# Optimization experiments

Hardware: AMD Instinct MI355X
Metric: run time of the kernel (lower is better)

## Reference

```python
import math
import jax, jax.numpy as jnp
import numpy as np

B, S, D, H = 2, 2048, 2048, 16
HD = D // H  # head_dim = 128


def setup_inputs() -> dict:
    key = jax.random.key(0)
    ks = jax.random.split(key, 5)
    x = jax.random.normal(ks[0], (B, S, D), dtype=jnp.float32)
    # torch nn.Linear weights are [out_features, in_features]
    wq = jax.random.normal(ks[1], (D, D), dtype=jnp.float32) * 0.02
    wk = jax.random.normal(ks[2], (D, D), dtype=jnp.float32) * 0.02
    wv = jax.random.normal(ks[3], (D, D), dtype=jnp.float32) * 0.02
    wo = jax.random.normal(ks[4], (D, D), dtype=jnp.float32) * 0.02
    # llama-style rotary frequencies: freq_cis[t, i] = exp(1j * t / 10000^(2i/hd))
    inv_freq = 1.0 / (10000.0 ** (jnp.arange(0, HD, 2, dtype=jnp.float32) / HD))  # [HD/2]
    angles = jnp.arange(S, dtype=jnp.float32)[:, None] * inv_freq[None, :]  # [S, HD/2]
    freq_cos = jnp.cos(angles)
    freq_sin = jnp.sin(angles)
    # additive causal mask (0 on/below diagonal, large negative above)
    mask = jnp.triu(jnp.full((S, S), -1e9, dtype=jnp.float32), k=1)
    return {"x": x, "wq": wq, "wk": wk, "wv": wv, "wo": wo,
            "freq_cos": freq_cos, "freq_sin": freq_sin, "mask": mask}


def _rope(t, cos, sin):
    # t: [B, H, S, HD]; cos/sin: [S, HD/2]. Consecutive pairs form complex numbers.
    b, h, s, hd = t.shape
    tr = t.reshape(b, h, s, hd // 2, 2)
    re, im = tr[..., 0], tr[..., 1]
    c = cos[None, None, :, :]
    sn = sin[None, None, :, :]
    out_re = re * c - im * sn
    out_im = re * sn + im * c
    return jnp.stack([out_re, out_im], axis=-1).reshape(b, h, s, hd)


def reference(x, wq, wk, wv, wo, freq_cos, freq_sin, mask):
    b, s, d = x.shape
    hd = 2 * freq_cos.shape[-1]
    h = wq.shape[0] // hd
    # projections (torch Linear: y = x @ W.T)
    q = jnp.einsum('bsd,ed->bse', x, wq).reshape(b, s, h, hd).transpose(0, 2, 1, 3)
    k = jnp.einsum('bsd,ed->bse', x, wk).reshape(b, s, h, hd).transpose(0, 2, 1, 3)
    v = jnp.einsum('bsd,ed->bse', x, wv).reshape(b, s, h, hd).transpose(0, 2, 1, 3)
    q = _rope(q, freq_cos, freq_sin)
    k = _rope(k, freq_cos, freq_sin)
    scores = jnp.einsum('bhqd,bhkd->bhqk', q, k) / math.sqrt(hd)  # [B,H,S,S]
    scores = scores + mask[None, None, :, :]
    attn = jax.nn.softmax(scores, axis=-1)
    o = jnp.einsum('bhqk,bhkd->bhqd', attn, v)
    o = o.transpose(0, 2, 1, 3).reshape(b, s, h * hd)
    return jnp.einsum('bse,de->bsd', o, wo)
```

## Files before the change

### kernel.cpp

```cpp
#include <hip/hip_runtime.h>
#include <stdint.h>

#define BB  2
#define SS  2048
#define DD  2048
#define HH  16
#define HDD 128
#define MM  (BB * SS)

typedef __attribute__((ext_vector_type(8)))  short short8;
typedef __attribute__((ext_vector_type(4)))  float f32x4;
typedef __attribute__((ext_vector_type(16))) float f32x16;
typedef unsigned int   u32;
typedef unsigned short u16;
typedef __attribute__((ext_vector_type(4))) u16 u16x4;
typedef __attribute__((ext_vector_type(2))) u32 u32x2;
typedef __attribute__((ext_vector_type(4))) u32 u32x4;

static __device__ __forceinline__ u16 f2bf(float f) {
  u32 u = __builtin_bit_cast(u32, f);
  u32 r = u + 0x7fffu + ((u >> 16) & 1u);
  return (u16)(r >> 16);
}

static __device__ __forceinline__ u32 cvtpk(float a, float b) {
  u32 r;
  asm("v_cvt_pk_bf16_f32 %0, %1, %2" : "=v"(r) : "v"(a), "v"(b));
  return r;
}
static __device__ __forceinline__ void permswap(u32& a, u32& b) {
  asm volatile("v_permlane32_swap_b32 %0, %1" : "+v"(a), "+v"(b));
}

__global__ void cvt_all(const float* __restrict__ x,  const float* __restrict__ wq,
                        const float* __restrict__ wk, const float* __restrict__ wv,
                        const float* __restrict__ wo,
                        u16* __restrict__ xb, u16* __restrict__ wqkv,
                        u16* __restrict__ wob) {
  const int NX = (MM * DD) / 4;
  const int NW = (DD * DD) / 4;
  const int total = NX + 4 * NW;
  for (int i = blockIdx.x * blockDim.x + threadIdx.x; i < total;
       i += gridDim.x * blockDim.x) {
    const float* s; u16* d; int off;
    if (i < NX) { s = x; d = xb; off = i; }
    else {
      int j = i - NX; int w = j >> 20; off = j & (NW - 1);
      s = (w == 0) ? wq : (w == 1) ? wk : (w == 2) ? wv : wo;
      d = (w < 3) ? (wqkv + (size_t)w * DD * DD) : wob;
    }
    f32x4 v = *(const f32x4*)(s + (size_t)off * 4);
    u16x4 o;
#pragma unroll
    for (int j = 0; j < 4; ++j) o[j] = f2bf(v[j]);
    *(u16x4*)(d + (size_t)off * 4) = o;
  }
}

__global__ __launch_bounds__(256) void gemm_qkv(const u16* __restrict__ A,
                                                const u16* __restrict__ Bw,
                                                u16* __restrict__ Cq,
                                                u16* __restrict__ Ck,
                                                u16* __restrict__ Cvt,
                                                const float* __restrict__ fc,
                                                const float* __restrict__ fs) {
  const int K = DD;
  __shared__ __align__(16) u16 Al[128 * 64];
  __shared__ __align__(16) u16 Bl[128 * 64];
  const int tid  = threadIdx.x;
  const int wave = tid >> 6, lane = tid & 63;
  const int m0 = blockIdx.y * 128, n0 = blockIdx.x * 128;
  const int wr = (wave >> 1) * 64, wc = (wave & 1) * 64;
  const int lrow = lane & 15, kh = lane >> 4;
  const int sk = lrow & 7;

  f32x4 acc[4][4] = {};

#define GSTAGE(T)                                                                       \
  {                                                                                     \
    int koff = (T) * 64;                                                                \
    _Pragma("unroll")                                                                   \
    for (int j_ = 0; j_ < 4; ++j_) {                                                    \
      int i_ = tid + j_ * 256;                                             \
      int r_ = i_ >> 3, c_ = i_ & 7;                                                    \
      int sc_ = (c_ ^ (r_ & 7)) * 8;                                                    \
      const u16* ga = A  + (size_t)(m0 + r_) * K + koff + sc_;                          \
      __builtin_amdgcn_global_load_lds((const __attribute__((address_space(1))) u32*)ga,\
                                       (__attribute__((address_space(3))) u32*)(Al + i_ * 8), \
                                       16, 0, 0);                                       \
      const u16* gb = Bw + (size_t)(n0 + r_) * K + koff + sc_;                          \
      __builtin_amdgcn_global_load_lds((const __attribute__((address_space(1))) u32*)gb,\
                                       (__attribute__((address_space(3))) u32*)(Bl + i_ * 8), \
                                       16, 0, 0);                                       \
    }                                                                                   \
  }

  const int NT = K / 64;
  for (int t = 0; t < NT; ++t) {
    if (t) __syncthreads();
    GSTAGE(t);
    __syncthreads();

    short8 af[4][2], bf[4][2];
#pragma unroll
    for (int tt = 0; tt < 4; ++tt)
#pragma unroll
      for (int ks = 0; ks < 2; ++ks) {
        af[tt][ks] = *(const short8*)(Al + (wr + tt * 16 + lrow) * 64 + ((ks * 4 + kh) ^ sk) * 8);
        bf[tt][ks] = *(const short8*)(Bl + (wc + tt * 16 + lrow) * 64 + ((ks * 4 + kh) ^ sk) * 8);
      }
#pragma unroll
    for (int mt = 0; mt < 4; ++mt)
#pragma unroll
      for (int nt = 0; nt < 4; ++nt)
#pragma unroll
        for (int ks = 0; ks < 2; ++ks)
          acc[mt][nt] = __builtin_amdgcn_mfma_f32_16x16x32_bf16(af[mt][ks], bf[nt][ks], acc[mt][nt], 0, 0, 0);
  }
#undef GSTAGE

  const int dr = kh * 4;
  const int region = n0 >> 11;
  if (region < 2) {
    u16* Cd = region ? Ck : Cq;
    const float sfac = region ? 1.f : 0.08838834764831845f * 1.44269504088896340736f;
#pragma unroll
    for (int mt = 0; mt < 4; ++mt)
#pragma unroll
      for (int nt = 0; nt < 4; ++nt) {
        int c  = n0 + wc + nt * 16 + lrow;
        int cl = c & 2047;
        int dh = cl & 127, pi = dh >> 1;
        float sgn = (dh & 1) ? 1.f : -1.f;
#pragma unroll
        for (int i = 0; i < 4; ++i) {
          int r  = m0 + wr + mt * 16 + dr + i;
          int s_ = r & (SS - 1);
          float cc_ = fc[s_ * 64 + pi] * sfac;
          float ss_ = fs[s_ * 64 + pi] * (sgn * sfac);
          float v  = acc[mt][nt][i];
          float pv = __shfl_xor(v, 1, 64);
          Cd[(size_t)r * 2048 + cl] = f2bf(v * cc_ + pv * ss_);
        }
      }
  } else {
#pragma unroll
    for (int mt = 0; mt < 4; ++mt)
#pragma unroll
      for (int nt = 0; nt < 4; ++nt) {
        int cl = (n0 - 4096) + wc + nt * 16 + lrow;
        int rr = m0 + wr + mt * 16 + dr;
        int b  = rr >> 11, s0 = rr & 2047;
        u16x4 pk;
#pragma unroll
        for (int i = 0; i < 4; ++i) pk[i] = f2bf(acc[mt][nt][i]);
        *(u16x4*)(Cvt + ((size_t)b * 2048 + cl) * 2048 + s0) = pk;
      }
  }
}

__global__ __launch_bounds__(256) void gemm_o_db(const u16* __restrict__ A,
                                                 const u16* __restrict__ Bw,
                                                 float* __restrict__ Cf,
                                                 int M, int N, int K) {
  __shared__ __align__(16) u16 Al[2][128 * 64];
  __shared__ __align__(16) u16 Bl[2][128 * 64];
  const int tid  = threadIdx.x;
  const int wave = tid >> 6, lane = tid & 63;
  const int m0 = blockIdx.y * 128, n0 = blockIdx.x * 128;
  const int wr = (wave >> 1) * 64, wc = (wave & 1) * 64;
  const int lrow = lane & 15, kh = lane >> 4;
  const int sk = lrow & 7;

  f32x4 acc[4][4] = {};

#define GSTAGE(T, BUF)                                                                  \
  {                                                                                     \
    int koff = (T) * 64;                                                                \
    _Pragma("unroll")                                                                   \
    for (int j_ = 0; j_ < 4; ++j_) {                                                    \
      int i_ = tid + j_ * 256;                                                          \
      int r_ = i_ >> 3, c_ = i_ & 7;                                                    \
      int sc_ = (c_ ^ (r_ & 7)) * 8;                                                    \
      const u16* ga = A  + (size_t)(m0 + r_) * K + koff + sc_;                          \
      __builtin_amdgcn_global_load_lds((const __attribute__((address_space(1))) u32*)ga,\
                                       (__attribute__((address_space(3))) u32*)(&Al[BUF][0] + i_ * 8), \
                                       16, 0, 0);                                       \
      const u16* gb = Bw + (size_t)(n0 + r_) * K + koff + sc_;                          \
      __builtin_amdgcn_global_load_lds((const __attribute__((address_space(1))) u32*)gb,\
                                       (__attribute__((address_space(3))) u32*)(&Bl[BUF][0] + i_ * 8), \
                                       16, 0, 0);                                       \
    }                                                                                   \
  }

  const int NT = K / 64;
  GSTAGE(0, 0);
  for (int t = 0; t < NT; ++t) {
    const int bt = t & 1;
    if (t + 1 < NT) {
      GSTAGE(t + 1, bt ^ 1);
      asm volatile("s_waitcnt vmcnt(8)" ::: "memory");
    } else {
      asm volatile("s_waitcnt vmcnt(0)" ::: "memory");
    }
    __builtin_amdgcn_s_barrier();

    const u16* Ab = &Al[bt][0];
    const u16* Bb = &Bl[bt][0];
    short8 af[4][2], bf[4][2];
#pragma unroll
    for (int tt = 0; tt < 4; ++tt)
#pragma unroll
      for (int ks = 0; ks < 2; ++ks) {
        af[tt][ks] = *(const short8*)(Ab + (wr + tt * 16 + lrow) * 64 + ((ks * 4 + kh) ^ sk) * 8);
        bf[tt][ks] = *(const short8*)(Bb + (wc + tt * 16 + lrow) * 64 + ((ks * 4 + kh) ^ sk) * 8);
      }
#pragma unroll
    for (int mt = 0; mt < 4; ++mt)
#pragma unroll
      for (int nt = 0; nt < 4; ++nt)
#pragma unroll
        for (int ks = 0; ks < 2; ++ks)
          acc[mt][nt] = __builtin_amdgcn_mfma_f32_16x16x32_bf16(af[mt][ks], bf[nt][ks], acc[mt][nt], 0, 0, 0);

    __builtin_amdgcn_s_barrier();
  }
#undef GSTAGE

  const int dr = kh * 4;
#pragma unroll
  for (int mt = 0; mt < 4; ++mt)
#pragma unroll
    for (int nt = 0; nt < 4; ++nt)
#pragma unroll
      for (int i = 0; i < 4; ++i) {
        size_t r = (size_t)(m0 + wr + mt * 16 + dr + i);
        size_t c = (size_t)(n0 + wc + nt * 16 + lrow);
        Cf[r * N + c] = acc[mt][nt][i];
      }
}

__global__ __launch_bounds__(256, 2) void attn_kernel(const u16* __restrict__ Q,
                                                      const u16* __restrict__ K,
                                                      const u16* __restrict__ Vt,
                                                      u16* __restrict__ O) {
  __shared__ __align__(16) u16 Kl[2][64 * 128];
  __shared__ __align__(16) u16 Vl[2][128 * 64];

  const int tid = threadIdx.x, wave = tid >> 6, lane = tid & 63;
  const int l31 = lane & 31, hi = lane >> 5;
  const int bh = blockIdx.x, b = bh >> 4, h = bh & 15;
  const int y = blockIdx.y;
  const int qt = (y < 8) ? y : (23 - y);
  const size_t base    = ((size_t)b * SS) * DD + (size_t)h * HDD;
  const size_t vt_base = (size_t)bh * HDD * SS;
  const int swz = (l31 & 7) << 4;

#define STAGE(KT, BUF)                                                              \
  {                                                                                 \
    int k0s = (KT) * 64;                                                            \
    _Pragma("unroll")                                                               \
    for (int i_ = 0; i_ < 4; ++i_) {                                                \
      int idx = tid + i_ * 256;                                                     \
      int kr = idx >> 4, c_ = idx & 15;                                             \
      const u16* gk = K + base + (size_t)(k0s + kr) * DD + ((c_ ^ (kr & 7)) * 8);   \
      __builtin_amdgcn_global_load_lds((const __attribute__((address_space(1))) u32*)gk, \
                                       (__attribute__((address_space(3))) u32*)(&Kl[BUF][0] + idx * 8), \
                                       16, 0, 0);                                   \
      int dv = idx >> 3, c2 = idx & 7;                                              \
      const u16* gv = Vt + vt_base + (size_t)dv * SS + k0s + ((c2 ^ (dv & 7)) * 8); \
      __builtin_amdgcn_global_load_lds((const __attribute__((address_space(1))) u32*)gv, \
                                       (__attribute__((address_space(3))) u32*)(&Vl[BUF][0] + idx * 8), \
                                       16, 0, 0);                                   \
    }                                                                               \
  }

  const int qw = qt * 128 + wave * 32;
  const int q_ = qw + l31;

  short8 qf[8];
#pragma unroll
  for (int kc = 0; kc < 8; ++kc)
    qf[kc] = *(const short8*)(Q + base + (size_t)(qw + l31) * DD + kc * 16 + hi * 8);

  f32x16 oacc[4] = {};
  float m_i = -1e30f, l_p = 0.f;

  int buf = 0;
  STAGE(0, 0);

  const int ntiles = 2 * qt + 2;
  for (int kt = 0; kt < ntiles; ++kt) {
    const int k0 = kt * 64;
    if (kt + 1 < ntiles) {
      STAGE(kt + 1, buf ^ 1);
      asm volatile("s_waitcnt vmcnt(8)" ::: "memory");
    } else {
      asm volatile("s_waitcnt vmcnt(0)" ::: "memory");
    }
    __builtin_amdgcn_s_barrier();

    if (k0 <= qw + 31) {
      const u16* Kb_ = &Kl[buf][0];
      const u16* Vb_ = &Vl[buf][0];

      f32x16 st[2] = {};
      __builtin_amdgcn_s_setprio(1);
#pragma unroll
      for (int kc = 0; kc < 8; ++kc) {
        int by0 = (l31 * 256)        + ((kc * 32 + hi * 16) ^ swz);
        int by1 = ((32 + l31) * 256) + ((kc * 32 + hi * 16) ^ swz);
        short8 a0 = *(const short8*)(Kb_ + (by0 >> 1));
        short8 a1 = *(const short8*)(Kb_ + (by1 >> 1));
        st[0] = __builtin_amdgcn_mfma_f32_32x32x16_bf16(a0, qf[kc], st[0], 0, 0, 0);
        st[1] = __builtin_amdgcn_mfma_f32_32x32x16_bf16(a1, qf[kc], st[1], 0, 0, 0);
      }
      __builtin_amdgcn_s_setprio(0);

      float mx = -1e30f;
      if (k0 + 63 > qw) {
#pragma unroll
        for (int kb = 0; kb < 2; ++kb)
#pragma unroll
          for (int r = 0; r < 16; ++r) {
            float s = st[kb][r];
            int key = k0 + kb * 32 + (r & 3) + ((r >> 2) << 3) + (hi << 2);
            if (key > q_) s = -1e30f;
            st[kb][r] = s;
            mx = fmaxf(mx, s);
          }
      } else {
#pragma unroll
        for (int kb = 0; kb < 2; ++kb)
#pragma unroll
          for (int r = 0; r < 16; ++r) mx = fmaxf(mx, st[kb][r]);
      }
      mx = fmaxf(mx, __shfl_xor(mx, 32, 64));

      if (__any(mx > m_i + 8.f)) {
        float mn  = fmaxf(m_i, mx);
        float esc = exp2f(m_i - mn);
        m_i = mn; l_p *= esc;
#pragma unroll
        for (int db = 0; db < 4; ++db)
#pragma unroll
          for (int r = 0; r < 16; ++r) oacc[db][r] *= esc;
      }
      float sum = 0.f;
#pragma unroll
      for (int kb = 0; kb < 2; ++kb)
#pragma unroll
        for (int r = 0; r < 16; ++r) {
          float e = exp2f(st[kb][r] - m_i);
          st[kb][r] = e;
          sum += e;
        }
      l_p += sum;

      __builtin_amdgcn_s_setprio(1);
#pragma unroll
      for (int kb = 0; kb < 2; ++kb) {
#pragma unroll
        for (int half = 0; half < 2; ++half) {
          const int rb = half * 8;
          u32 w0 = cvtpk(st[kb][rb + 0], st[kb][rb + 1]);
          u32 w1 = cvtpk(st[kb][rb + 2], st[kb][rb + 3]);
          u32 w2 = cvtpk(st[kb][rb + 4], st[kb][rb + 5]);
          u32 w3 = cvtpk(st[kb][rb + 6], st[kb][rb + 7]);
          permswap(w0, w2);
          permswap(w1, w3);
          short8 pf = __builtin_bit_cast(short8, (u32x4){w0, w1, w2, w3});
          const int ktv = kb * 2 + half;
#pragma unroll
          for (int db = 0; db < 4; ++db) {
            int d = db * 32 + l31;
            int by = d * 128 + ((ktv * 32 + hi * 16) ^ swz);
            short8 vf = *(const short8*)(Vb_ + (by >> 1));
            oacc[db] = __builtin_amdgcn_mfma_f32_32x32x16_bf16(vf, pf, oacc[db], 0, 0, 0);
          }
        }
      }
      __builtin_amdgcn_s_setprio(0);
    }
    __builtin_amdgcn_s_barrier();
    buf ^= 1;
  }

  float lt  = l_p + __shfl_xor(l_p, 32, 64);
  float inv = 1.f / lt;
#pragma unroll
  for (int db = 0; db < 4; ++db)
#pragma unroll
    for (int g = 0; g < 4; ++g) {
      int d0 = db * 32 + 8 * g + 4 * hi;
      u32x2 pk;
      pk[0] = cvtpk(oacc[db][4 * g + 0] * inv, oacc[db][4 * g + 1] * inv);
      pk[1] = cvtpk(oacc[db][4 * g + 2] * inv, oacc[db][4 * g + 3] * inv);
      *(u32x2*)(O + base + (size_t)q_ * DD + d0) = pk;
    }
#undef STAGE
}

extern "C" void kernel_launch(void* const* d_in, const int* in_sizes, int n_in,
                              void* d_out, int out_size, void* d_ws, size_t ws_size,
                              hipStream_t stream) {
  (void)in_sizes; (void)n_in; (void)out_size; (void)ws_size;
  const float* x  = (const float*)d_in[0];
  const float* wq = (const float*)d_in[1];
  const float* wk = (const float*)d_in[2];
  const float* wv = (const float*)d_in[3];
  const float* wo = (const float*)d_in[4];
  const float* fc = (const float*)d_in[5];
  const float* fs = (const float*)d_in[6];
  float* out = (float*)d_out;

  const size_t XBUF = (size_t)MM * DD * 2;
  const size_t WBUF = (size_t)DD * DD * 2;
  char* ws = (char*)d_ws;
  u16* xb   = (u16*)(ws);
  u16* Qb   = (u16*)(ws + XBUF);
  u16* Kb   = (u16*)(ws + 2 * XBUF);
  u16* Vtb  = (u16*)(ws + 3 * XBUF);
  u16* wqkv = (u16*)(ws + 4 * XBUF);
  u16* wob  = (u16*)(ws + 4 * XBUF + 3 * WBUF);
  u16* Ob   = xb;

  cvt_all<<<2048, 256, 0, stream>>>(x, wq, wk, wv, wo, xb, wqkv, wob);

  gemm_qkv<<<dim3(48, 32), 256, 0, stream>>>(xb, wqkv, Qb, Kb, Vtb, fc, fs);

  attn_kernel<<<dim3(32, 16), 256, 0, stream>>>(Qb, Kb, Vtb, Ob);

  gemm_o_db<<<dim3(16, 32), 256, 0, stream>>>(Ob, wob, out, MM, DD, DD);
}
```

Measured before the change: 246.4 us.

## Shrink output-projection GEMM tile to 128x64 and drop double buffering

Replaces the double-buffered 128x128 output-projection GEMM with a single-buffered 128x64 tile, doubling the grid from 512 to 1024 blocks. Each wave now computes a 64x32 sub-tile, and loads are synchronised with __syncthreads before compute. The aim is more blocks for better CU fill on the 4096x2048 GEMM and lower LDS/register use for higher occupancy. In exchange it loses the overlap of global loads with MFMA work and reloads more A data per output element.

```diff
diff --git a/kernel.cpp b/kernel.cpp
--- a/kernel.cpp
+++ b/kernel.cpp
@@ -159,71 +159,70 @@
   }
 }
 
-__global__ __launch_bounds__(256) void gemm_o_db(const u16* __restrict__ A,
-                                                 const u16* __restrict__ Bw,
-                                                 float* __restrict__ Cf,
-                                                 int M, int N, int K) {
-  __shared__ __align__(16) u16 Al[2][128 * 64];
-  __shared__ __align__(16) u16 Bl[2][128 * 64];
+__global__ __launch_bounds__(256) void gemm_o(const u16* __restrict__ A,
+                                              const u16* __restrict__ Bw,
+                                              float* __restrict__ Cf,
+                                              int M, int N, int K) {
+  __shared__ __align__(16) u16 Al[128 * 64];
+  __shared__ __align__(16) u16 Bl[64 * 64];
   const int tid  = threadIdx.x;
   const int wave = tid >> 6, lane = tid & 63;
-  const int m0 = blockIdx.y * 128, n0 = blockIdx.x * 128;
-  const int wr = (wave >> 1) * 64, wc = (wave & 1) * 64;
+  const int m0 = blockIdx.y * 128, n0 = blockIdx.x * 64;
+  const int wr = (wave >> 1) * 64, wc = (wave & 1) * 32;
   const int lrow = lane & 15, kh = lane >> 4;
   const int sk = lrow & 7;
 
-  f32x4 acc[4][4] = {};
-
-#define GSTAGE(T, BUF)                                                                  \
+  f32x4 acc[4][2] = {};
+
+#define GSTAGE(T)                                                                       \
   {                                                                                     \
     int koff = (T) * 64;                                                                \
     _Pragma("unroll")                                                                   \
-    for (int j_ = 0; j_ < 4; ++j_) {                                                    \
+    for (int j_ = 0; j_ < 4; ++j_) {                                \
       int i_ = tid + j_ * 256;                                                          \
       int r_ = i_ >> 3, c_ = i_ & 7;                                                    \
       int sc_ = (c_ ^ (r_ & 7)) * 8;                                                    \
-      const u16* ga = A  + (size_t)(m0 + r_) * K + koff + sc_;                          \
+      const u16* ga = A + (size_t)(m0 + r_) * K + koff + sc_;                           \
       __builtin_amdgcn_global_load_lds((const __attribute__((address_space(1))) u32*)ga,\
-                                       (__attribute__((address_space(3))) u32*)(&Al[BUF][0] + i_ * 8), \
+                                       (__attribute__((address_space(3))) u32*)(Al + i_ * 8), \
                                        16, 0, 0);                                       \
+    }                                                                                   \
+    _Pragma("unroll")                                                                   \
+    for (int j_ = 0; j_ < 2; ++j_) {                                 \
+      int ib = tid + j_ * 256;                                                          \
+      int r_ = ib >> 3, c_ = ib & 7;                                                    \
+      int sc_ = (c_ ^ (r_ & 7)) * 8;                                                    \
       const u16* gb = Bw + (size_t)(n0 + r_) * K + koff + sc_;                          \
       __builtin_amdgcn_global_load_lds((const __attribute__((address_space(1))) u32*)gb,\
-                                       (__attribute__((address_space(3))) u32*)(&Bl[BUF][0] + i_ * 8), \
+                                       (__attribute__((address_space(3))) u32*)(Bl + ib * 8), \
                                        16, 0, 0);                                       \
     }                                                                                   \
   }
 
   const int NT = K / 64;
-  GSTAGE(0, 0);
   for (int t = 0; t < NT; ++t) {
-    const int bt = t & 1;
-    if (t + 1 < NT) {
-      GSTAGE(t + 1, bt ^ 1);
-      asm volatile("s_waitcnt vmcnt(8)" ::: "memory");
-    } else {
-      asm volatile("s_waitcnt vmcnt(0)" ::: "memory");
-    }
-    __builtin_amdgcn_s_barrier();
-
-    const u16* Ab = &Al[bt][0];
-    const u16* Bb = &Bl[bt][0];
-    short8 af[4][2], bf[4][2];
+    if (t) __syncthreads();
+    GSTAGE(t);
+    __syncthreads();
+
+    short8 af[4][2], bf[2][2];
 #pragma unroll
     for (int tt = 0; tt < 4; ++tt)
 #pragma unroll
-      for (int ks = 0; ks < 2; ++ks) {
-        af[tt][ks] = *(const short8*)(Ab + (wr + tt * 16 + lrow) * 64 + ((ks * 4 + kh) ^ sk) * 8);
-        bf[tt][ks] = *(const short8*)(Bb + (wc + tt * 16 + lrow) * 64 + ((ks * 4 + kh) ^ sk) * 8);
-      }
+      for (int ks = 0; ks < 2; ++ks)
+        af[tt][ks] = *(const short8*)(Al + (wr + tt * 16 + lrow) * 64 + ((ks * 4 + kh) ^ sk) * 8);
+#pragma unroll
+    for (int g = 0; g < 2; ++g)
+#pragma unroll
+      for (int ks = 0; ks < 2; ++ks)
+        bf[g][ks] = *(const short8*)(Bl + (wc + g * 16 + lrow) * 64 + ((ks * 4 + kh) ^ sk) * 8);
 #pragma unroll
     for (int mt = 0; mt < 4; ++mt)
 #pragma unroll
-      for (int nt = 0; nt < 4; ++nt)
+      for (int nt = 0; nt < 2; ++nt)
 #pragma unroll
         for (int ks = 0; ks < 2; ++ks)
           acc[mt][nt] = __builtin_amdgcn_mfma_f32_16x16x32_bf16(af[mt][ks], bf[nt][ks], acc[mt][nt], 0, 0, 0);
-
-    __builtin_amdgcn_s_barrier();
   }
 #undef GSTAGE
 
@@ -231,7 +230,7 @@
 #pragma unroll
   for (int mt = 0; mt < 4; ++mt)
 #pragma unroll
-    for (int nt = 0; nt < 4; ++nt)
+    for (int nt = 0; nt < 2; ++nt)
 #pragma unroll
       for (int i = 0; i < 4; ++i) {
         size_t r = (size_t)(m0 + wr + mt * 16 + dr + i);
@@ -431,5 +430,5 @@
 
   attn_kernel<<<dim3(32, 16), 256, 0, stream>>>(Qb, Kb, Vtb, Ob);
 
-  gemm_o_db<<<dim3(16, 32), 256, 0, stream>>>(Ob, wob, out, MM, DD, DD);
-}
+  gemm_o<<<dim3(32, 32), 256, 0, stream>>>(Ob, wob, out, MM, DD, DD);
+}
```

Result: no change. 247.0 us (+0.2%).
